# Kernel optimization log

Hardware: AMD Instinct MI355X
Metric: run time of the kernel (lower is better)

Reference implementation:

```python
import jax, jax.numpy as jnp
import numpy as np

IN_NUM, IN_DIM = 1152, 8
OUT_NUM, OUT_DIM = 10, 16
BATCH = 256
NUM_ROUTING = 3


def setup_inputs() -> dict:
    key = jax.random.key(0)
    k1, k2 = jax.random.split(key)
    x = jax.random.normal(k1, (BATCH, IN_DIM, IN_NUM), dtype=jnp.float32)
    W = jax.random.normal(k2, (IN_NUM, OUT_NUM, OUT_DIM, IN_DIM), dtype=jnp.float32)
    return {"x": x, "W": W}


def squash(s):
    # s: [out_num, batch, out_dim]; squash along capsule dim (axis=2)
    mag_sq = jnp.sum(s * s, axis=2, keepdims=True)
    mag = jnp.sqrt(mag_sq)
    return mag_sq / (1.0 + mag_sq) * (s / mag)


def reference(x, W):
    # u_hat[i,j,b,o] = sum_d W[i,j,o,d] * x[b,d,i]  -> [in_num, out_num, batch, out_dim]
    u_hat = jnp.einsum('ijod,bdi->ijbo', W, x)
    batch = x.shape[0]
    b_ij = jnp.zeros((IN_NUM, OUT_NUM), dtype=u_hat.dtype)
    v = None
    for _ in range(NUM_ROUTING):
        # DGL mailbox is [out, in]; softmax(dim=0) == softmax over output capsules j
        c = jax.nn.softmax(b_ij, axis=1)                 # [in, out]
        s = jnp.einsum('ij,ijbo->jbo', c, u_hat)          # [out, batch, out_dim]
        v = squash(s)                                     # [out, batch, out_dim]
        # edge update: b_ij += (v_j . u_hat_ij) summed over dim, averaged over batch
        b_ij = b_ij + jnp.einsum('jbo,ijbo->ij', v, u_hat) / batch
    return v
```

## Files before the change

### kernel.cpp

```cpp
#include <hip/hip_runtime.h>
#include <math.h>

#define IN_NUM 1152
#define IN_DIM 8
#define OUT_NUM 10
#define OUT_DIM 16
#define BATCH 256
#define KTOT 9216
#define WJ 147456

typedef __attribute__((ext_vector_type(8))) short short8;
typedef __attribute__((ext_vector_type(4))) float f32x4;

__device__ __forceinline__ unsigned short f2bf(float f) {
    unsigned int u = __builtin_bit_cast(unsigned int, f);
    u += 0x7FFF + ((u >> 16) & 1);
    return (unsigned short)(u >> 16);
}
__device__ __forceinline__ float bf2f(unsigned short h) {
    unsigned int u = ((unsigned int)h) << 16;
    return __builtin_bit_cast(float, u);
}

__global__ __launch_bounds__(256) void k_prep_w(const float* __restrict__ W,
                                                unsigned short* __restrict__ Wo) {
    const int j  = blockIdx.x / 18;
    const int i0 = (blockIdx.x % 18) * 64;
    __shared__ float Ls[128][65];
    const int t = threadIdx.x;
    #pragma unroll 4
    for (int st = 0; st < 32; ++st) {
        const int il = st * 2 + (t >> 7);
        const int od = t & 127;
        Ls[od][il] = W[(size_t)(i0 + il) * 1280 + j * 128 + od];
    }
    __syncthreads();
    #pragma unroll 4
    for (int st = 0; st < 32; ++st) {
        const int od = st * 4 + (t >> 6);
        const int il = t & 63;
        const int o = od >> 3, d = od & 7;
        Wo[(size_t)j * WJ + o * KTOT + d * IN_NUM + i0 + il] = f2bf(Ls[od][il]);
    }
}

__global__ __launch_bounds__(256) void k_prep_x(const float* __restrict__ x,
                                                unsigned short* __restrict__ xb,
                                                unsigned short* __restrict__ xT) {
    const int k0 = blockIdx.x * 64;
    const int b0 = blockIdx.y * 64;
    __shared__ float Xs[64][65];
    const int t = threadIdx.x;
    #pragma unroll 4
    for (int st = 0; st < 16; ++st) {
        const int bl = st * 4 + (t >> 6);
        const int kl = t & 63;
        const float f = x[(size_t)(b0 + bl) * KTOT + k0 + kl];
        Xs[kl][bl] = f;
        xb[(size_t)(b0 + bl) * KTOT + k0 + kl] = f2bf(f);
    }
    __syncthreads();
    #pragma unroll 4
    for (int st = 0; st < 16; ++st) {
        const int kl = st * 4 + (t >> 6);
        const int bl = t & 63;
        xT[(size_t)(k0 + kl) * BATCH + b0 + bl] = f2bf(Xs[kl][bl]);
    }
}

__global__ __launch_bounds__(256) void k_softmax(const float* __restrict__ b,
                                                 float* __restrict__ Ct) {
    const int i = blockIdx.x * blockDim.x + threadIdx.x;
    if (i >= IN_NUM) return;
    float v[OUT_NUM];
    float m = -INFINITY;
    for (int j = 0; j < OUT_NUM; ++j) { v[j] = b[i * OUT_NUM + j]; m = fmaxf(m, v[j]); }
    float ssum = 0.f;
    for (int j = 0; j < OUT_NUM; ++j) { v[j] = expf(v[j] - m); ssum += v[j]; }
    const float inv = 1.0f / ssum;
    for (int j = 0; j < OUT_NUM; ++j) Ct[j * IN_NUM + i] = v[j] * inv;
}

__global__ __launch_bounds__(256) void k_wc(const unsigned short* __restrict__ Wo,
                                            const float* __restrict__ Ct,
                                            unsigned short* __restrict__ Wc) {
    const size_t f = ((size_t)blockIdx.x * 256 + threadIdx.x) * 8;
    const int j  = (int)(f / WJ);
    const int r1 = (int)(f % WJ);
    const int i  = r1 % IN_NUM;
    const unsigned short* wp = Wo + f;
    const float* cp = Ct + j * IN_NUM + i;
    unsigned short out[8];
    #pragma unroll
    for (int e = 0; e < 8; ++e) out[e] = f2bf(bf2f(wp[e]) * cp[e]);
    *reinterpret_cast<short8*>(Wc + f) = *reinterpret_cast<const short8*>(out);
}

__global__ __launch_bounds__(256) void k_gemm_s(const unsigned short* __restrict__ A,
                                                const unsigned short* __restrict__ xb,
                                                float* __restrict__ s) {
    const int wid  = blockIdx.x * 4 + (threadIdx.x >> 6);
    const int lane = threadIdx.x & 63;
    const int kc    = wid & 15;
    const int btile = (wid >> 4) & 15;
    const int j     = wid >> 8;
    const int row = lane & 15, kg = lane >> 4;

    const unsigned short* ap = A  + (size_t)j * WJ + row * KTOT + kc * 576 + kg * 8;
    const unsigned short* bp = xb + (size_t)(btile * 16 + row) * KTOT + kc * 576 + kg * 8;

    f32x4 acc = {0.f, 0.f, 0.f, 0.f};
    #pragma unroll
    for (int t = 0; t < 18; ++t) {
        short8 a = *reinterpret_cast<const short8*>(ap);
        short8 b = *reinterpret_cast<const short8*>(bp);
        acc = __builtin_amdgcn_mfma_f32_16x16x32_bf16(a, b, acc, 0, 0, 0);
        ap += 32; bp += 32;
    }
    float* sp = s + (size_t)j * OUT_DIM * BATCH + (kg * 4) * BATCH + btile * 16 + row;
    atomicAdd(sp + 0 * BATCH, acc[0]);
    atomicAdd(sp + 1 * BATCH, acc[1]);
    atomicAdd(sp + 2 * BATCH, acc[2]);
    atomicAdd(sp + 3 * BATCH, acc[3]);
}

__global__ __launch_bounds__(256) void k_squash(const float* __restrict__ s,
                                                unsigned short* __restrict__ vb,
                                                float* __restrict__ out,
                                                float scale, int write_out) {
    const int j = blockIdx.x, b = threadIdx.x;
    const float* sp = s + (size_t)j * OUT_DIM * BATCH + b;
    float sv[OUT_DIM];
    float m2 = 0.f;
    #pragma unroll
    for (int o = 0; o < OUT_DIM; ++o) { sv[o] = sp[o * BATCH] * scale; m2 += sv[o] * sv[o]; }
    const float f = sqrtf(m2) / (1.0f + m2);
    unsigned short* vp = vb + (size_t)j * OUT_DIM * BATCH + b;
    #pragma unroll
    for (int o = 0; o < OUT_DIM; ++o) vp[o * BATCH] = f2bf(sv[o] * f);
    if (write_out) {
        float* op = out + ((size_t)j * BATCH + b) * OUT_DIM;
        #pragma unroll
        for (int o = 0; o < OUT_DIM; ++o) op[o] = sv[o] * f;
    }
}

__global__ __launch_bounds__(256) void k_gemm_G(const unsigned short* __restrict__ xT,
                                                const unsigned short* __restrict__ vb,
                                                float* __restrict__ G) {
    const int wid  = blockIdx.x * 4 + (threadIdx.x >> 6);
    const int lane = threadIdx.x & 63;
    const int j  = wid % 10;
    const int kt = wid / 10;
    const int rc = lane & 15, kg = lane >> 4;

    const unsigned short* ap = xT + (size_t)(kt * 16 + rc) * BATCH + kg * 8;
    const unsigned short* bp = vb + (size_t)j * OUT_DIM * BATCH + rc * BATCH + kg * 8;

    f32x4 acc = {0.f, 0.f, 0.f, 0.f};
    #pragma unroll
    for (int bb = 0; bb < 8; ++bb) {
        short8 a = *reinterpret_cast<const short8*>(ap + bb * 32);
        short8 b = *reinterpret_cast<const short8*>(bp + bb * 32);
        acc = __builtin_amdgcn_mfma_f32_16x16x32_bf16(a, b, acc, 0, 0, 0);
    }
    float* gp = G + (size_t)j * WJ + (size_t)(kt * 16 + kg * 4) * OUT_DIM + rc;
    #pragma unroll
    for (int r = 0; r < 4; ++r) gp[r * OUT_DIM] = acc[r];
}

__global__ __launch_bounds__(256) void k_bupdate(const float* __restrict__ W,
                                                 const float* __restrict__ G,
                                                 float* __restrict__ b) {
    const int p = blockIdx.x * 256 + threadIdx.x;
    const int j = p / IN_NUM, i = p - j * IN_NUM;
    const float* Wp = W + (size_t)i * 1280 + j * 128;
    const float* Gj = G + (size_t)j * WJ;
    float acc = 0.f;
    #pragma unroll
    for (int d = 0; d < IN_DIM; ++d) {
        const float* gr = Gj + (size_t)(d * IN_NUM + i) * OUT_DIM;
        float4 g0 = *reinterpret_cast<const float4*>(gr + 0);
        float4 g1 = *reinterpret_cast<const float4*>(gr + 4);
        float4 g2 = *reinterpret_cast<const float4*>(gr + 8);
        float4 g3 = *reinterpret_cast<const float4*>(gr + 12);
        acc += Wp[0 * 8 + d] * g0.x + Wp[1 * 8 + d] * g0.y
             + Wp[2 * 8 + d] * g0.z + Wp[3 * 8 + d] * g0.w
             + Wp[4 * 8 + d] * g1.x + Wp[5 * 8 + d] * g1.y
             + Wp[6 * 8 + d] * g1.z + Wp[7 * 8 + d] * g1.w
             + Wp[8 * 8 + d] * g2.x + Wp[9 * 8 + d] * g2.y
             + Wp[10 * 8 + d] * g2.z + Wp[11 * 8 + d] * g2.w
             + Wp[12 * 8 + d] * g3.x + Wp[13 * 8 + d] * g3.y
             + Wp[14 * 8 + d] * g3.z + Wp[15 * 8 + d] * g3.w;
    }
    b[i * OUT_NUM + j] += acc * (1.0f / BATCH);
}

extern "C" void kernel_launch(void* const* d_in, const int* in_sizes, int n_in,
                              void* d_out, int out_size, void* d_ws, size_t ws_size,
                              hipStream_t stream) {
    const float* x = (const float*)d_in[0];
    const float* W = (const float*)d_in[1];
    float* out = (float*)d_out;
    float* ws = (float*)d_ws;

    float*          b  = ws;
    float*          Ct = ws + 11520;
    float*          s  = ws + 23040;
    float*          G  = ws + 64000;
    unsigned short* Wo = (unsigned short*)(ws + 1538560);
    unsigned short* Wc = (unsigned short*)(ws + 2275840);
    unsigned short* xb = (unsigned short*)(ws + 3013120);
    unsigned short* xT = (unsigned short*)(ws + 4192768);
    unsigned short* vb = (unsigned short*)(ws + 5372416);

    hipMemsetAsync(b, 0, (size_t)IN_NUM * OUT_NUM * sizeof(float), stream);
    k_prep_w<<<180, 256, 0, stream>>>(W, Wo);
    k_prep_x<<<dim3(144, 4), 256, 0, stream>>>(x, xb, xT);

    for (int it = 0; it < 3; ++it) {
        const unsigned short* A = Wo;
        if (it > 0) {
            k_softmax<<<5, 256, 0, stream>>>(b, Ct);
            k_wc<<<720, 256, 0, stream>>>(Wo, Ct, Wc);
            A = Wc;
        }
        hipMemsetAsync(s, 0, (size_t)OUT_NUM * OUT_DIM * BATCH * sizeof(float), stream);
        k_gemm_s<<<640, 256, 0, stream>>>(A, xb, s);
        k_squash<<<OUT_NUM, BATCH, 0, stream>>>(s, vb, out,
                                                it == 0 ? 0.1f : 1.0f, it == 2 ? 1 : 0);
        if (it < 2) {
            k_gemm_G<<<1440, 256, 0, stream>>>(xT, vb, G);
            k_bupdate<<<45, 256, 0, stream>>>(W, G, b);
        }
    }
}
```

Baseline: 131.1 us.

## Fuse GEMM with squash, fold b-update into G GEMM, merge prep kernels

The two prep kernels become one launch. The s-GEMM now reduces its split-K partials in shared memory inside a block and applies squash directly, which removes the atomics, the memsets and the separate squash kernel. The G GEMM multiplies by bf16 W and shuffle-reduces in its epilogue to write per-d partial logits, replacing the large fp32 G buffer and the bupdate kernel. The softmax kernel now also sums those partials and accumulates the logits. The cost is fewer s-GEMM blocks (160) with a longer K loop each, and W in the b-update is bf16 instead of fp32.

```diff
diff --git a/kernel.cpp b/kernel.cpp
--- a/kernel.cpp
+++ b/kernel.cpp
@@ -10,6 +10,7 @@
 #define WJ 147456
 
 typedef __attribute__((ext_vector_type(8))) short short8;
+typedef __attribute__((ext_vector_type(4))) short short4v;
 typedef __attribute__((ext_vector_type(4))) float f32x4;
 
 __device__ __forceinline__ unsigned short f2bf(float f) {
@@ -22,63 +23,157 @@
     return __builtin_bit_cast(float, u);
 }
 
-__global__ __launch_bounds__(256) void k_prep_w(const float* __restrict__ W,
-                                                unsigned short* __restrict__ Wo) {
-    const int j  = blockIdx.x / 18;
-    const int i0 = (blockIdx.x % 18) * 64;
-    __shared__ float Ls[128][65];
+__global__ __launch_bounds__(256) void k_prep(const float* __restrict__ W,
+                                              const float* __restrict__ x,
+                                              unsigned short* __restrict__ Wo,
+                                              unsigned short* __restrict__ xb,
+                                              unsigned short* __restrict__ xT) {
+    __shared__ float Ls[128 * 65];
     const int t = threadIdx.x;
-    #pragma unroll 4
-    for (int st = 0; st < 32; ++st) {
-        const int il = st * 2 + (t >> 7);
-        const int od = t & 127;
-        Ls[od][il] = W[(size_t)(i0 + il) * 1280 + j * 128 + od];
-    }
+    if (blockIdx.x < 180) {
+        const int j  = blockIdx.x / 18;
+        const int i0 = (blockIdx.x % 18) * 64;
+        #pragma unroll 4
+        for (int st = 0; st < 32; ++st) {
+            const int il = st * 2 + (t >> 7);
+            const int od = t & 127;
+            Ls[il * 130 + od] = W[(size_t)(i0 + il) * 1280 + j * 128 + od];
+        }
+        __syncthreads();
+        #pragma unroll 4
+        for (int st = 0; st < 32; ++st) {
+            const int od = st * 4 + (t >> 6);
+            const int il = t & 63;
+            const int o = od >> 3, d = od & 7;
+            Wo[(size_t)j * WJ + o * KTOT + d * IN_NUM + i0 + il] = f2bf(Ls[il * 130 + od]);
+        }
+    } else {
+        const int bx = blockIdx.x - 180;
+        const int k0 = (bx >> 2) * 64;
+        const int b0 = (bx & 3) * 64;
+        #pragma unroll 4
+        for (int st = 0; st < 16; ++st) {
+            const int bl = st * 4 + (t >> 6);
+            const int kl = t & 63;
+            const float f = x[(size_t)(b0 + bl) * KTOT + k0 + kl];
+            Ls[kl * 65 + bl] = f;
+            xb[(size_t)(b0 + bl) * KTOT + k0 + kl] = f2bf(f);
+        }
+        __syncthreads();
+        #pragma unroll 4
+        for (int st = 0; st < 16; ++st) {
+            const int kl = st * 4 + (t >> 6);
+            const int bl = t & 63;
+            xT[(size_t)(k0 + kl) * BATCH + b0 + bl] = f2bf(Ls[kl * 65 + bl]);
+        }
+    }
+}
+
+__global__ __launch_bounds__(256) void k_gemm_sq(const unsigned short* __restrict__ A,
+                                                 const unsigned short* __restrict__ xb,
+                                                 unsigned short* __restrict__ vb,
+                                                 float* __restrict__ out,
+                                                 float scale, int wout) {
+    const int j     = blockIdx.x >> 4;
+    const int btile = blockIdx.x & 15;
+    const int w    = threadIdx.x >> 6;
+    const int lane = threadIdx.x & 63;
+    const int row = lane & 15, kg = lane >> 4;
+
+    const unsigned short* ap = A  + (size_t)j * WJ + row * KTOT + w * 2304 + kg * 8;
+    const unsigned short* bp = xb + (size_t)(btile * 16 + row) * KTOT + w * 2304 + kg * 8;
+
+    f32x4 acc = {0.f, 0.f, 0.f, 0.f};
+    #pragma unroll 8
+    for (int it = 0; it < 72; ++it) {
+        short8 a = *reinterpret_cast<const short8*>(ap);
+        short8 b = *reinterpret_cast<const short8*>(bp);
+        acc = __builtin_amdgcn_mfma_f32_16x16x32_bf16(a, b, acc, 0, 0, 0);
+        ap += 32; bp += 32;
+    }
+    __shared__ float Sred[4][16][16];
+    __shared__ float fs[16];
+    #pragma unroll
+    for (int r = 0; r < 4; ++r) Sred[w][kg * 4 + r][row] = acc[r];
     __syncthreads();
-    #pragma unroll 4
-    for (int st = 0; st < 32; ++st) {
-        const int od = st * 4 + (t >> 6);
-        const int il = t & 63;
-        const int o = od >> 3, d = od & 7;
-        Wo[(size_t)j * WJ + o * KTOT + d * IN_NUM + i0 + il] = f2bf(Ls[od][il]);
-    }
-}
-
-__global__ __launch_bounds__(256) void k_prep_x(const float* __restrict__ x,
-                                                unsigned short* __restrict__ xb,
-                                                unsigned short* __restrict__ xT) {
-    const int k0 = blockIdx.x * 64;
-    const int b0 = blockIdx.y * 64;
-    __shared__ float Xs[64][65];
-    const int t = threadIdx.x;
-    #pragma unroll 4
-    for (int st = 0; st < 16; ++st) {
-        const int bl = st * 4 + (t >> 6);
-        const int kl = t & 63;
-        const float f = x[(size_t)(b0 + bl) * KTOT + k0 + kl];
-        Xs[kl][bl] = f;
-        xb[(size_t)(b0 + bl) * KTOT + k0 + kl] = f2bf(f);
-    }
+
+    const int o = threadIdx.x >> 4, b = threadIdx.x & 15;
+    float sum = Sred[0][o][b] + Sred[1][o][b] + Sred[2][o][b] + Sred[3][o][b];
+    Sred[0][o][b] = sum;
     __syncthreads();
-    #pragma unroll 4
-    for (int st = 0; st < 16; ++st) {
-        const int kl = st * 4 + (t >> 6);
-        const int bl = t & 63;
-        xT[(size_t)(k0 + kl) * BATCH + b0 + bl] = f2bf(Xs[kl][bl]);
-    }
-}
-
-__global__ __launch_bounds__(256) void k_softmax(const float* __restrict__ b,
-                                                 float* __restrict__ Ct) {
+    float m2r = 0.f;
+    #pragma unroll
+    for (int oo = 0; oo < 16; ++oo) { const float q = Sred[0][oo][b]; m2r += q * q; }
+    const float m2 = m2r * scale * scale;
+    const float f  = sqrtf(m2) / (1.0f + m2);
+    vb[(size_t)j * OUT_DIM * BATCH + o * BATCH + btile * 16 + b] = f2bf(sum * scale * f);
+    if (wout) {
+        if (o == 0) fs[b] = f;
+        __syncthreads();
+        const int b2 = threadIdx.x >> 4, o2 = threadIdx.x & 15;
+        out[((size_t)j * BATCH + btile * 16 + b2) * OUT_DIM + o2] =
+            Sred[0][o2][b2] * scale * fs[b2];
+    }
+}
+
+__global__ __launch_bounds__(256) void k_gemm_Gb(const unsigned short* __restrict__ xT,
+                                                 const unsigned short* __restrict__ vb,
+                                                 const unsigned short* __restrict__ Wo,
+                                                 float* __restrict__ bp) {
+    const int wid  = blockIdx.x * 4 + (threadIdx.x >> 6);
+    const int lane = threadIdx.x & 63;
+    const int j  = wid % 10;
+    const int kt = wid / 10;
+    const int rc = lane & 15, kg = lane >> 4;
+
+    const unsigned short* ap = xT + (size_t)(kt * 16 + rc) * BATCH + kg * 8;
+    const unsigned short* vp = vb + (size_t)j * OUT_DIM * BATCH + rc * BATCH + kg * 8;
+
+    f32x4 acc = {0.f, 0.f, 0.f, 0.f};
+    #pragma unroll
+    for (int bb = 0; bb < 8; ++bb) {
+        short8 a = *reinterpret_cast<const short8*>(ap + bb * 32);
+        short8 b = *reinterpret_cast<const short8*>(vp + bb * 32);
+        acc = __builtin_amdgcn_mfma_f32_16x16x32_bf16(a, b, acc, 0, 0, 0);
+    }
+    const int kbase = kt * 16 + kg * 4;
+    short4v w4 = *reinterpret_cast<const short4v*>(
+        Wo + (size_t)j * WJ + rc * KTOT + kbase);
+    float p[4];
+    #pragma unroll
+    for (int r = 0; r < 4; ++r) p[r] = acc[r] * bf2f((unsigned short)w4[r]);
+    #pragma unroll
+    for (int m = 1; m < 16; m <<= 1) {
+        #pragma unroll
+        for (int r = 0; r < 4; ++r) p[r] += __shfl_xor(p[r], m);
+    }
+    if (rc == 0) {
+        float4 v4 = make_float4(p[0], p[1], p[2], p[3]);
+        *reinterpret_cast<float4*>(bp + (size_t)j * KTOT + kbase) = v4;
+    }
+}
+
+__global__ __launch_bounds__(256) void k_softmaxb(const float* __restrict__ bp,
+                                                  float* __restrict__ blog,
+                                                  float* __restrict__ Ct,
+                                                  int first) {
     const int i = blockIdx.x * blockDim.x + threadIdx.x;
     if (i >= IN_NUM) return;
-    float v[OUT_NUM];
+    float lg[OUT_NUM];
     float m = -INFINITY;
-    for (int j = 0; j < OUT_NUM; ++j) { v[j] = b[i * OUT_NUM + j]; m = fmaxf(m, v[j]); }
+    for (int j = 0; j < OUT_NUM; ++j) {
+        float a = first ? 0.f : blog[i * OUT_NUM + j];
+        float s = 0.f;
+        #pragma unroll
+        for (int d = 0; d < IN_DIM; ++d) s += bp[(size_t)j * KTOT + d * IN_NUM + i];
+        a += s * (1.0f / BATCH);
+        lg[j] = a; blog[i * OUT_NUM + j] = a;
+        m = fmaxf(m, a);
+    }
     float ssum = 0.f;
-    for (int j = 0; j < OUT_NUM; ++j) { v[j] = expf(v[j] - m); ssum += v[j]; }
+    for (int j = 0; j < OUT_NUM; ++j) { lg[j] = expf(lg[j] - m); ssum += lg[j]; }
     const float inv = 1.0f / ssum;
-    for (int j = 0; j < OUT_NUM; ++j) Ct[j * IN_NUM + i] = v[j] * inv;
+    for (int j = 0; j < OUT_NUM; ++j) Ct[j * IN_NUM + i] = lg[j] * inv;
 }
 
 __global__ __launch_bounds__(256) void k_wc(const unsigned short* __restrict__ Wo,
@@ -86,114 +181,13 @@
                                             unsigned short* __restrict__ Wc) {
     const size_t f = ((size_t)blockIdx.x * 256 + threadIdx.x) * 8;
     const int j  = (int)(f / WJ);
-    const int r1 = (int)(f % WJ);
-    const int i  = r1 % IN_NUM;
+    const int i  = (int)(f % WJ) % IN_NUM;
     const unsigned short* wp = Wo + f;
     const float* cp = Ct + j * IN_NUM + i;
-    unsigned short out[8];
-    #pragma unroll
-    for (int e = 0; e < 8; ++e) out[e] = f2bf(bf2f(wp[e]) * cp[e]);
-    *reinterpret_cast<short8*>(Wc + f) = *reinterpret_cast<const short8*>(out);
-}
-
-__global__ __launch_bounds__(256) void k_gemm_s(const unsigned short* __restrict__ A,
-                                                const unsigned short* __restrict__ xb,
-                                                float* __restrict__ s) {
-    const int wid  = blockIdx.x * 4 + (threadIdx.x >> 6);
-    const int lane = threadIdx.x & 63;
-    const int kc    = wid & 15;
-    const int btile = (wid >> 4) & 15;
-    const int j     = wid >> 8;
-    const int row = lane & 15, kg = lane >> 4;
-
-    const unsigned short* ap = A  + (size_t)j * WJ + row * KTOT + kc * 576 + kg * 8;
-    const unsigned short* bp = xb + (size_t)(btile * 16 + row) * KTOT + kc * 576 + kg * 8;
-
-    f32x4 acc = {0.f, 0.f, 0.f, 0.f};
-    #pragma unroll
-    for (int t = 0; t < 18; ++t) {
-        short8 a = *reinterpret_cast<const short8*>(ap);
-        short8 b = *reinterpret_cast<const short8*>(bp);
-        acc = __builtin_amdgcn_mfma_f32_16x16x32_bf16(a, b, acc, 0, 0, 0);
-        ap += 32; bp += 32;
-    }
-    float* sp = s + (size_t)j * OUT_DIM * BATCH + (kg * 4) * BATCH + btile * 16 + row;
-    atomicAdd(sp + 0 * BATCH, acc[0]);
-    atomicAdd(sp + 1 * BATCH, acc[1]);
-    atomicAdd(sp + 2 * BATCH, acc[2]);
-    atomicAdd(sp + 3 * BATCH, acc[3]);
-}
-
-__global__ __launch_bounds__(256) void k_squash(const float* __restrict__ s,
-                                                unsigned short* __restrict__ vb,
-                                                float* __restrict__ out,
-                                                float scale, int write_out) {
-    const int j = blockIdx.x, b = threadIdx.x;
-    const float* sp = s + (size_t)j * OUT_DIM * BATCH + b;
-    float sv[OUT_DIM];
-    float m2 = 0.f;
-    #pragma unroll
-    for (int o = 0; o < OUT_DIM; ++o) { sv[o] = sp[o * BATCH] * scale; m2 += sv[o] * sv[o]; }
-    const float f = sqrtf(m2) / (1.0f + m2);
-    unsigned short* vp = vb + (size_t)j * OUT_DIM * BATCH + b;
-    #pragma unroll
-    for (int o = 0; o < OUT_DIM; ++o) vp[o * BATCH] = f2bf(sv[o] * f);
-    if (write_out) {
-        float* op = out + ((size_t)j * BATCH + b) * OUT_DIM;
-        #pragma unroll
-        for (int o = 0; o < OUT_DIM; ++o) op[o] = sv[o] * f;
-    }
-}
-
-__global__ __launch_bounds__(256) void k_gemm_G(const unsigned short* __restrict__ xT,
-                                                const unsigned short* __restrict__ vb,
-                                                float* __restrict__ G) {
-    const int wid  = blockIdx.x * 4 + (threadIdx.x >> 6);
-    const int lane = threadIdx.x & 63;
-    const int j  = wid % 10;
-    const int kt = wid / 10;
-    const int rc = lane & 15, kg = lane >> 4;
-
-    const unsigned short* ap = xT + (size_t)(kt * 16 + rc) * BATCH + kg * 8;
-    const unsigned short* bp = vb + (size_t)j * OUT_DIM * BATCH + rc * BATCH + kg * 8;
-
-    f32x4 acc = {0.f, 0.f, 0.f, 0.f};
-    #pragma unroll
-    for (int bb = 0; bb < 8; ++bb) {
-        short8 a = *reinterpret_cast<const short8*>(ap + bb * 32);
-        short8 b = *reinterpret_cast<const short8*>(bp + bb * 32);
-        acc = __builtin_amdgcn_mfma_f32_16x16x32_bf16(a, b, acc, 0, 0, 0);
-    }
-    float* gp = G + (size_t)j * WJ + (size_t)(kt * 16 + kg * 4) * OUT_DIM + rc;
-    #pragma unroll
-    for (int r = 0; r < 4; ++r) gp[r * OUT_DIM] = acc[r];
-}
-
-__global__ __launch_bounds__(256) void k_bupdate(const float* __restrict__ W,
-                                                 const float* __restrict__ G,
-                                                 float* __restrict__ b) {
-    const int p = blockIdx.x * 256 + threadIdx.x;
-    const int j = p / IN_NUM, i = p - j * IN_NUM;
-    const float* Wp = W + (size_t)i * 1280 + j * 128;
-    const float* Gj = G + (size_t)j * WJ;
-    float acc = 0.f;
-    #pragma unroll
-    for (int d = 0; d < IN_DIM; ++d) {
-        const float* gr = Gj + (size_t)(d * IN_NUM + i) * OUT_DIM;
-        float4 g0 = *reinterpret_cast<const float4*>(gr + 0);
-        float4 g1 = *reinterpret_cast<const float4*>(gr + 4);
-        float4 g2 = *reinterpret_cast<const float4*>(gr + 8);
-        float4 g3 = *reinterpret_cast<const float4*>(gr + 12);
-        acc += Wp[0 * 8 + d] * g0.x + Wp[1 * 8 + d] * g0.y
-             + Wp[2 * 8 + d] * g0.z + Wp[3 * 8 + d] * g0.w
-             + Wp[4 * 8 + d] * g1.x + Wp[5 * 8 + d] * g1.y
-             + Wp[6 * 8 + d] * g1.z + Wp[7 * 8 + d] * g1.w
-             + Wp[8 * 8 + d] * g2.x + Wp[9 * 8 + d] * g2.y
-             + Wp[10 * 8 + d] * g2.z + Wp[11 * 8 + d] * g2.w
-             + Wp[12 * 8 + d] * g3.x + Wp[13 * 8 + d] * g3.y
-             + Wp[14 * 8 + d] * g3.z + Wp[15 * 8 + d] * g3.w;
-    }
-    b[i * OUT_NUM + j] += acc * (1.0f / BATCH);
+    unsigned short outv[8];
+    #pragma unroll
+    for (int e = 0; e < 8; ++e) outv[e] = f2bf(bf2f(wp[e]) * cp[e]);
+    *reinterpret_cast<short8*>(Wc + f) = *reinterpret_cast<const short8*>(outv);
 }
 
 extern "C" void kernel_launch(void* const* d_in, const int* in_sizes, int n_in,
@@ -204,34 +198,26 @@
     float* out = (float*)d_out;
     float* ws = (float*)d_ws;
 
-    float*          b  = ws;
-    float*          Ct = ws + 11520;
-    float*          s  = ws + 23040;
-    float*          G  = ws + 64000;
-    unsigned short* Wo = (unsigned short*)(ws + 1538560);
-    unsigned short* Wc = (unsigned short*)(ws + 2275840);
-    unsigned short* xb = (unsigned short*)(ws + 3013120);
-    unsigned short* xT = (unsigned short*)(ws + 4192768);
-    unsigned short* vb = (unsigned short*)(ws + 5372416);
-
-    hipMemsetAsync(b, 0, (size_t)IN_NUM * OUT_NUM * sizeof(float), stream);
-    k_prep_w<<<180, 256, 0, stream>>>(W, Wo);
-    k_prep_x<<<dim3(144, 4), 256, 0, stream>>>(x, xb, xT);
-
-    for (int it = 0; it < 3; ++it) {
-        const unsigned short* A = Wo;
-        if (it > 0) {
-            k_softmax<<<5, 256, 0, stream>>>(b, Ct);
-            k_wc<<<720, 256, 0, stream>>>(Wo, Ct, Wc);
-            A = Wc;
-        }
-        hipMemsetAsync(s, 0, (size_t)OUT_NUM * OUT_DIM * BATCH * sizeof(float), stream);
-        k_gemm_s<<<640, 256, 0, stream>>>(A, xb, s);
-        k_squash<<<OUT_NUM, BATCH, 0, stream>>>(s, vb, out,
-                                                it == 0 ? 0.1f : 1.0f, it == 2 ? 1 : 0);
-        if (it < 2) {
-            k_gemm_G<<<1440, 256, 0, stream>>>(xT, vb, G);
-            k_bupdate<<<45, 256, 0, stream>>>(W, G, b);
-        }
-    }
-}
+    float*          blog = ws;
+    float*          Ct   = ws + 11520;
+    float*          bpb  = ws + 23040;
+    unsigned short* vb   = (unsigned short*)(ws + 115200);
+    unsigned short* Wo   = (unsigned short*)(ws + 135680);
+    unsigned short* Wc   = (unsigned short*)(ws + 872960);
+    unsigned short* xb   = (unsigned short*)(ws + 1610240);
+    unsigned short* xT   = (unsigned short*)(ws + 2789888);
+
+    k_prep<<<756, 256, 0, stream>>>(W, x, Wo, xb, xT);
+
+    k_gemm_sq<<<160, 256, 0, stream>>>(Wo, xb, vb, out, 0.1f, 0);
+    k_gemm_Gb<<<1440, 256, 0, stream>>>(xT, vb, Wo, bpb);
+
+    k_softmaxb<<<5, 256, 0, stream>>>(bpb, blog, Ct, 1);
+    k_wc<<<720, 256, 0, stream>>>(Wo, Ct, Wc);
+    k_gemm_sq<<<160, 256, 0, stream>>>(Wc, xb, vb, out, 1.0f, 0);
+    k_gemm_Gb<<<1440, 256, 0, stream>>>(xT, vb, Wo, bpb);
+
+    k_softmaxb<<<5, 256, 0, stream>>>(bpb, blog, Ct, 0);
+    k_wc<<<720, 256, 0, stream>>>(Wo, Ct, Wc);
+    k_gemm_sq<<<160, 256, 0, stream>>>(Wc, xb, vb, out, 1.0f, 1);
+}
```

Result: faster. 112.5 us (-14.2%).
